# Performance work log

Hardware: AMD Instinct MI355X
Metric: run time of the kernel (lower is better)

Reference implementation:

```python
import jax, jax.numpy as jnp
import numpy as np

NB, BS, NHID, NINP = 6, 200, 1200, 2400  # num_blocks, block_size, nhid, ninp (=2*nhid)
T, B, NTOK = 32, 32, 16000


def _ln(x, g, b):
    mu = x.mean(-1, keepdims=True)
    v = ((x - mu) ** 2).mean(-1, keepdims=True)
    return (x - mu) / jnp.sqrt(v + 1e-5) * g + b


def _attend(q3, k3, v3, wq, wk, wv, wfc, g, b, nh, dk, dv, residual):
    # q3/k3/v3: (B, L, d_model); multi-head scaled-dot attention across blocks
    Bz, L, _ = q3.shape
    qh = (q3 @ wq).reshape(Bz, L, nh, dk)
    kh = (k3 @ wk).reshape(Bz, L, nh, dk)
    vh = (v3 @ wv).reshape(Bz, L, nh, dv)
    att = jnp.einsum('bqhd,bkhd->bhqk', qh, kh) / float(np.sqrt(dk))
    att = jax.nn.softmax(att, axis=-1)
    out = jnp.einsum('bhqk,bkhd->bqhd', att, vh).reshape(Bz, L, nh * dv)
    out = out @ wfc
    if residual:
        out = out + q3
    return _ln(out, g, b)


def setup_inputs() -> dict:
    key = jax.random.key(0)
    ks = jax.random.split(key, 16)
    rn = lambda i, sh, s: jax.random.normal(ks[i], sh, dtype=jnp.float32) * s
    d = {}
    d['tokens'] = jax.random.randint(ks[0], (T, B), 0, NTOK)
    d['h0'] = jnp.zeros((2, B, NHID), jnp.float32)
    d['c0'] = jnp.zeros((2, B, NHID), jnp.float32)
    d['emb_table'] = jax.random.uniform(ks[1], (NTOK, NINP), jnp.float32, -0.1, 0.1)
    d['Wi'] = rn(2, (NB, 4 * BS, NINP), 0.01)
    d['Wh'] = rn(3, (NB, 4 * BS, BS), 0.05)
    d['bih'] = jnp.zeros((NB, 4 * BS), jnp.float32)
    d['bhh'] = jnp.zeros((NB, 4 * BS), jnp.float32)
    d['mq'] = rn(4, (BS, 64), 0.07)
    d['mk'] = rn(5, (BS, 64), 0.07)
    d['mv'] = rn(6, (BS, 64), 0.07)
    d['mfc'] = rn(7, (64, BS), 0.1)
    d['mg'] = jnp.ones((BS,), jnp.float32)
    d['mb'] = jnp.zeros((BS,), jnp.float32)
    d['lq'] = rn(8, (BS, 1600), 0.07)
    d['lk'] = rn(9, (BS, 1600), 0.07)
    d['lv'] = rn(10, (BS, 1600), 0.07)
    d['lfc'] = rn(11, (1600, 2400), 0.02)
    d['lg'] = jnp.ones((2400,), jnp.float32)
    d['lb'] = jnp.zeros((2400,), jnp.float32)
    d['dec_w'] = jax.random.uniform(ks[12], (NTOK, NHID), jnp.float32, -0.1, 0.1)
    d['dec_b'] = jnp.zeros((NTOK,), jnp.float32)
    return d


def reference(tokens, h0, c0, emb_table, Wi, Wh, bih, bhh, mq, mk, mv, mfc, mg, mb,
              lq, lk, lv, lfc, lg, lb, dec_w, dec_b):
    def block_lstm(x, h, c):
        # block-diagonal LSTMCell: k independent cells, per-block input NINP, hidden BS
        Bz = x.shape[0]
        xb = x.reshape(Bz, NB, -1)
        hb = h.reshape(Bz, NB, BS)
        cb = c.reshape(Bz, NB, BS)
        gt = jnp.einsum('bki,kgi->bkg', xb, Wi) + jnp.einsum('bkh,kgh->bkg', hb, Wh) + bih + bhh
        ii, ff, gg, oo = jnp.split(gt, 4, axis=-1)  # torch LSTMCell gate order i,f,g,o
        cn = jax.nn.sigmoid(ff) * cb + jax.nn.sigmoid(ii) * jnp.tanh(gg)
        hn = jax.nn.sigmoid(oo) * jnp.tanh(cn)
        return hn.reshape(Bz, NHID), cn.reshape(Bz, NHID)

    def self_att(h):
        hb = h.reshape(-1, NB, BS)
        hb = _attend(hb, hb, hb, mq, mk, mv, mfc, mg, mb, 4, 16, 16, True)
        return hb.reshape(-1, NHID)

    emb = emb_table[tokens]  # (T, B, NINP)

    def step0(carry, x):
        h, c = carry
        h, c = block_lstm(jnp.tile(x, (1, NB)), h, c)
        h = self_att(h)
        return (h, c), h

    (hf0, cf0), out = jax.lax.scan(step0, (h0[0], c0[0]), emb)

    def step1(carry, x):
        h, c = carry
        q = h.reshape(-1, NB, BS)
        kv = x.reshape(-1, NB, BS)
        inp = _attend(q, kv, kv, lq, lk, lv, lfc, lg, lb, 8, BS, BS, False)  # (B, NB, 2400)
        h, c = block_lstm(inp.reshape(inp.shape[0], -1), h, c)
        h = self_att(h)
        return (h, c), h

    (hf1, cf1), out = jax.lax.scan(step1, (h0[1], c0[1]), out)

    decoded = out @ dec_w.T + dec_b  # (T, B, NTOK)
    return decoded, jnp.stack([hf0, hf1]), jnp.stack([cf0, cf1])
```

## Files before the change

kernel.cpp:

```cpp
#include <hip/hip_runtime.h>
#include <math.h>

#define NBLK 6
#define BS   200
#define NHID 1200
#define NINP 2400
#define TT   32
#define BZ   32
#define NTOK 16000
#define NG   4800
#define ROWS 1024
#define L1D  1600
#define ST   (BZ*NHID)

__device__ __forceinline__ float sigmoidf_(float x) { return 1.0f / (1.0f + expf(-x)); }

template <bool BT>
__global__ __launch_bounds__(256) void gemm128_kernel(
    const float* __restrict__ A, const float* __restrict__ B,
    const float* __restrict__ bias1, const float* __restrict__ bias2,
    float* __restrict__ C, int M, int N, int K, const int* __restrict__ a_idx)
{
    __shared__ __align__(16) float As[8][132];
    __shared__ __align__(16) float Bs[8][132];
    const int tid = threadIdx.x;
    const int tx = tid & 15, ty = tid >> 4;
    const int n0 = blockIdx.x * 128, m0 = blockIdx.y * 128;

    const int la_r = tid >> 1, la_k = (tid & 1) * 4;
    long arow;
    {
        int row = m0 + la_r;
        arow = a_idx ? (long)a_idx[row] * K : (long)row * K;
    }
    float acc[8][8] = {};

    for (int k0 = 0; k0 < K; k0 += 8) {
        {
            float4 v = *(const float4*)&A[arow + k0 + la_k];
            As[la_k + 0][la_r] = v.x;
            As[la_k + 1][la_r] = v.y;
            As[la_k + 2][la_r] = v.z;
            As[la_k + 3][la_r] = v.w;
        }
        if constexpr (!BT) {
            int kk = tid >> 5, n = (tid & 31) * 4;
            int col = n0 + n;
            float4 v = make_float4(0.f, 0.f, 0.f, 0.f);
            if (col < N) v = *(const float4*)&B[(long)(k0 + kk) * N + col];
            *(float4*)&Bs[kk][n] = v;
        } else {
            int n = tid >> 1, kk0 = (tid & 1) * 4;
            int col = n0 + n;
            float4 v = make_float4(0.f, 0.f, 0.f, 0.f);
            if (col < N) v = *(const float4*)&B[(long)col * K + k0 + kk0];
            Bs[kk0 + 0][n] = v.x;
            Bs[kk0 + 1][n] = v.y;
            Bs[kk0 + 2][n] = v.z;
            Bs[kk0 + 3][n] = v.w;
        }
        __syncthreads();
        #pragma unroll
        for (int kk = 0; kk < 8; kk++) {
            float av[8], bv[8];
            *(float4*)&av[0] = *(const float4*)&As[kk][ty * 4];
            *(float4*)&av[4] = *(const float4*)&As[kk][ty * 4 + 64];
            *(float4*)&bv[0] = *(const float4*)&Bs[kk][tx * 4];
            *(float4*)&bv[4] = *(const float4*)&Bs[kk][tx * 4 + 64];
            #pragma unroll
            for (int i = 0; i < 8; i++)
                #pragma unroll
                for (int j = 0; j < 8; j++) acc[i][j] += av[i] * bv[j];
        }
        __syncthreads();
    }
    #pragma unroll
    for (int i = 0; i < 8; i++) {
        int row = m0 + ty * 4 + (i & 3) + (i >> 2) * 64;
        #pragma unroll
        for (int jg = 0; jg < 2; jg++) {
            int col = n0 + tx * 4 + jg * 64;
            if (col < N) {
                float4 v;
                v.x = acc[i][jg * 4 + 0]; v.y = acc[i][jg * 4 + 1];
                v.z = acc[i][jg * 4 + 2]; v.w = acc[i][jg * 4 + 3];
                if (bias1) {
                    float4 b1 = *(const float4*)&bias1[col];
                    v.x += b1.x; v.y += b1.y; v.z += b1.z; v.w += b1.w;
                }
                if (bias2) {
                    float4 b2 = *(const float4*)&bias2[col];
                    v.x += b2.x; v.y += b2.y; v.z += b2.z; v.w += b2.w;
                }
                *(float4*)&C[(long)row * N + col] = v;
            }
        }
    }
}

__global__ __launch_bounds__(256) void gemm_skp_kernel(
    const float* __restrict__ A, const float* __restrict__ B,
    float* __restrict__ Cp, int M, int N, int K, int KL)
{
    __shared__ __align__(16) float As[8][68];
    __shared__ __align__(16) float Bs[8][68];
    const int tid = threadIdx.x;
    const int tx = tid & 15, ty = tid >> 4;
    const int n0 = blockIdx.x * 64, m0 = blockIdx.y * 64;
    const int z = blockIdx.z;
    const int kbeg = z * KL, kend = kbeg + KL;

    float acc[4][4] = {};

    for (int k0 = kbeg; k0 < kend; k0 += 8) {
        {
            int idx = tid * 2;
            int mm = idx >> 3, kk = idx & 7;
            int row = m0 + mm;
            float2 v = *(const float2*)&A[(long)row * K + k0 + kk];
            As[kk][mm] = v.x;
            As[kk + 1][mm] = v.y;
        }
        {
            int idx = tid * 2;
            int nn = idx & 63, kk = idx >> 6;
            int n = n0 + nn;
            float2 v = make_float2(0.f, 0.f);
            if (n < N) v = *(const float2*)&B[(long)(k0 + kk) * N + n];
            Bs[kk][nn] = v.x;
            Bs[kk][nn + 1] = v.y;
        }
        __syncthreads();
        #pragma unroll
        for (int kk = 0; kk < 8; kk++) {
            const float4 a4 = *(const float4*)&As[kk][ty * 4];
            const float4 b4 = *(const float4*)&Bs[kk][tx * 4];
            const float av[4] = {a4.x, a4.y, a4.z, a4.w};
            const float bv[4] = {b4.x, b4.y, b4.z, b4.w};
            #pragma unroll
            for (int i = 0; i < 4; i++)
                #pragma unroll
                for (int j = 0; j < 4; j++) acc[i][j] += av[i] * bv[j];
        }
        __syncthreads();
    }
    float* Cz = Cp + (long)z * M * N;
    #pragma unroll
    for (int i = 0; i < 4; i++) {
        int row = m0 + ty * 4 + i;
        #pragma unroll
        for (int j = 0; j < 4; j++) {
            int col = n0 + tx * 4 + j;
            if (col < N) Cz[(long)row * N + col] = acc[i][j];
        }
    }
}

__global__ __launch_bounds__(256) void bigb_kernel(
    const float* __restrict__ lq, const float* __restrict__ lk,
    float* __restrict__ BigB)
{
    int id = blockIdx.x * 256 + threadIdx.x;
    if (id >= 320000) return;
    int h = id / 40000, r = id % 40000, cp = r / 200, c = r % 200;
    const float4* a = (const float4*)(lq + (long)c * L1D + h * 200);
    const float4* b = (const float4*)(lk + (long)cp * L1D + h * 200);
    float s0 = 0, s1 = 0, s2 = 0, s3 = 0;
    #pragma unroll 5
    for (int d = 0; d < 50; d++) {
        float4 av = a[d], bv = b[d];
        s0 += av.x * bv.x; s1 += av.y * bv.y; s2 += av.z * bv.z; s3 += av.w * bv.w;
    }
    BigB[(long)cp * L1D + h * 200 + c] = s0 + s1 + s2 + s3;
}

__global__ __launch_bounds__(256) void whT_kernel(
    const float* __restrict__ Wh, float* __restrict__ WhT)
{
    int id = blockIdx.x * 256 + threadIdx.x;
    if (id >= 960000) return;
    int k = id / 160000, r = id % 160000, m = r / 800, g = r % 800;
    WhT[id] = Wh[(long)(k * 800 + g) * 200 + m];
}

__device__ __forceinline__ void att_inline(
    float* hb, float* aux, float* gout,
    const float* __restrict__ mq, const float* __restrict__ mk,
    const float* __restrict__ mv, const float* __restrict__ mfc,
    const float* __restrict__ mg, const float* __restrict__ mb)
{
    const int tid = threadIdx.x;
    float* qh   = aux;
    float* kh   = aux + 384;
    float* vh   = aux + 768;
    float* att  = aux + 1152;
    float* outp = aux + 1296;
    float* o2   = aux + 1680;
    float* mu_s = aux + 2880;
    float* rs_s = aux + 2888;
    if (tid < 192) {
        int which = tid >> 6, hd = tid & 63;
        const float* Mw = which == 0 ? mq : (which == 1 ? mk : mv);
        float acc[6] = {};
        for (int jx = 0; jx < 200; jx++) {
            float w = Mw[jx * 64 + hd];
            #pragma unroll
            for (int l = 0; l < 6; l++) acc[l] += hb[l * 200 + jx] * w;
        }
        float* dst = which == 0 ? qh : (which == 1 ? kh : vh);
        #pragma unroll
        for (int l = 0; l < 6; l++) dst[l * 64 + hd] = acc[l];
    }
    __syncthreads();
    if (tid < 144) {
        int h = tid / 36, r = tid % 36, q = r / 6, kk = r % 6;
        float s = 0;
        #pragma unroll
        for (int d = 0; d < 16; d++) s += qh[q * 64 + h * 16 + d] * kh[kk * 64 + h * 16 + d];
        att[(h * 6 + q) * 6 + kk] = s * 0.25f;
    }
    __syncthreads();
    if (tid < 24) {
        float* a = att + tid * 6;
        float mx = a[0];
        for (int i = 1; i < 6; i++) mx = fmaxf(mx, a[i]);
        float sm = 0;
        for (int i = 0; i < 6; i++) { a[i] = expf(a[i] - mx); sm += a[i]; }
        float inv = 1.f / sm;
        for (int i = 0; i < 6; i++) a[i] *= inv;
    }
    __syncthreads();
    for (int id = tid; id < 384; id += 256) {
        int q = id >> 6, hd = id & 63, h = hd >> 4;
        float s = 0;
        #pragma unroll
        for (int kk = 0; kk < 6; kk++) s += att[(h * 6 + q) * 6 + kk] * vh[kk * 64 + hd];
        outp[id] = s;
    }
    __syncthreads();
    if (tid < 200) {
        float acc[6] = {};
        for (int d = 0; d < 64; d++) {
            float w = mfc[d * 200 + tid];
            #pragma unroll
            for (int q = 0; q < 6; q++) acc[q] += outp[q * 64 + d] * w;
        }
        #pragma unroll
        for (int q = 0; q < 6; q++) o2[q * 200 + tid] = acc[q] + hb[q * 200 + tid];
    }
    __syncthreads();
    if (tid < 6) {
        const float4* o4 = (const float4*)(o2 + tid * 200);
        float s = 0, s2 = 0;
        for (int i = 0; i < 50; i++) {
            float4 v = o4[i];
            s += v.x + v.y + v.z + v.w;
            s2 += v.x * v.x + v.y * v.y + v.z * v.z + v.w * v.w;
        }
        float mu = s / 200.f;
        float var = s2 / 200.f - mu * mu;
        mu_s[tid] = mu;
        rs_s[tid] = 1.0f / sqrtf(var + 1e-5f);
    }
    __syncthreads();
    for (int i = tid; i < 300; i += 256) {
        int q = i / 50;
        float4 v = ((float4*)o2)[i];
        float4 g4 = ((const float4*)mg)[i % 50];
        float4 b4 = ((const float4*)mb)[i % 50];
        float mu = mu_s[q], rstd = rs_s[q];
        float4 r;
        r.x = (v.x - mu) * rstd * g4.x + b4.x;
        r.y = (v.y - mu) * rstd * g4.y + b4.y;
        r.z = (v.z - mu) * rstd * g4.z + b4.z;
        r.w = (v.w - mu) * rstd * g4.w + b4.w;
        ((float4*)hb)[i] = r;
        if (gout) ((float4*)(gout))[i] = r;
    }
    __syncthreads();
}

__global__ __launch_bounds__(256) void phaseA_kernel(
    const float* __restrict__ GX0, const float* __restrict__ h0,
    const float* __restrict__ c0, const float* __restrict__ WhT,
    float* __restrict__ out0, float* __restrict__ cf0,
    const float* __restrict__ mq, const float* __restrict__ mk,
    const float* __restrict__ mv, const float* __restrict__ mfc,
    const float* __restrict__ mg, const float* __restrict__ mb)
{
    __shared__ __align__(16) float h_s[1200];
    __shared__ __align__(16) float c_s[1200];
    __shared__ __align__(16) float g_s[4800];
    __shared__ __align__(16) float gx_s[4800];
    __shared__ __align__(16) float aux[2896];
    const int b = blockIdx.x, tid = threadIdx.x;
    for (int i = tid; i < 300; i += 256) {
        ((float4*)h_s)[i] = ((const float4*)(h0 + b * NHID))[i];
        ((float4*)c_s)[i] = ((const float4*)(c0 + b * NHID))[i];
    }
    __syncthreads();
    for (int t = 0; t < TT; t++) {
        const float4* gx4 = (const float4*)(GX0 + ((long)t * BZ + b) * NG);
        for (int i = tid; i < 1200; i += 256) ((float4*)gx_s)[i] = gx4[i];
        if (tid < 200) {
            #pragma unroll
            for (int k = 0; k < 6; k++) {
                const float* wp = WhT + (long)k * 160000 + tid * 4;
                float a0 = 0, a1 = 0, a2 = 0, a3 = 0;
                for (int m = 0; m < 200; m++) {
                    float hv = h_s[k * 200 + m];
                    float4 w = *(const float4*)(wp + (long)m * 800);
                    a0 += hv * w.x; a1 += hv * w.y; a2 += hv * w.z; a3 += hv * w.w;
                }
                int gb = k * 800 + tid * 4;
                g_s[gb] = a0; g_s[gb + 1] = a1; g_s[gb + 2] = a2; g_s[gb + 3] = a3;
            }
        }
        __syncthreads();
        for (int idx = tid; idx < 1200; idx += 256) {
            int k = idx / 200, j = idx - k * 200;
            int base = k * 800 + j;
            float gi = g_s[base] + gx_s[base];
            float gf = g_s[base + 200] + gx_s[base + 200];
            float gg = g_s[base + 400] + gx_s[base + 400];
            float go = g_s[base + 600] + gx_s[base + 600];
            float cn = sigmoidf_(gf) * c_s[idx] + sigmoidf_(gi) * tanhf(gg);
            c_s[idx] = cn;
            h_s[idx] = sigmoidf_(go) * tanhf(cn);
        }
        __syncthreads();
        att_inline(h_s, aux, out0 + (long)t * ST + b * NHID, mq, mk, mv, mfc, mg, mb);
    }
    for (int i = tid; i < 300; i += 256)
        ((float4*)(cf0 + b * NHID))[i] = ((float4*)c_s)[i];
}

template <bool FIRST>
__global__ __launch_bounds__(256) void fusedatt_kernel(
    const float* __restrict__ htmp, const float* __restrict__ h0l1,
    float* __restrict__ out1_prev,
    const float* __restrict__ KMt, const float* __restrict__ VHt,
    float* __restrict__ attV,
    const float* __restrict__ mq, const float* __restrict__ mk,
    const float* __restrict__ mv, const float* __restrict__ mfc,
    const float* __restrict__ mg, const float* __restrict__ mb)
{
    __shared__ __align__(16) float hb[1200];
    __shared__ __align__(16) float aux[2896];
    __shared__ float attp[72];
    __shared__ float attr[36];
    const int blk = blockIdx.x, b = blk >> 3, h = blk & 7, tid = threadIdx.x;
    if (FIRST) {
        for (int i = tid; i < 300; i += 256)
            ((float4*)hb)[i] = ((const float4*)(h0l1 + b * NHID))[i];
        __syncthreads();
    } else {
        for (int i = tid; i < 300; i += 256)
            ((float4*)hb)[i] = ((const float4*)(htmp + b * NHID))[i];
        __syncthreads();
        att_inline(hb, aux, (h == 0) ? out1_prev + b * NHID : nullptr,
                   mq, mk, mv, mfc, mg, mb);
    }
    const float* kb = KMt + (long)b * 9600 + h * 200;
    if (tid < 72) {
        int r = tid >> 1, half = tid & 1;
        int q = r / 6, kk = r % 6;
        const float4* qr = (const float4*)(hb + q * 200 + half * 100);
        const float4* kr = (const float4*)(kb + (long)kk * L1D + half * 100);
        float s0 = 0, s1 = 0, s2 = 0, s3 = 0;
        #pragma unroll 5
        for (int d = 0; d < 25; d++) {
            float4 a = qr[d], v = kr[d];
            s0 += a.x * v.x; s1 += a.y * v.y; s2 += a.z * v.z; s3 += a.w * v.w;
        }
        attp[tid] = s0 + s1 + s2 + s3;
    }
    __syncthreads();
    if (tid < 6) {
        float v[6]; float mx = -1e30f;
        #pragma unroll
        for (int kk = 0; kk < 6; kk++) {
            float s = (attp[(tid * 6 + kk) * 2] + attp[(tid * 6 + kk) * 2 + 1]) * 0.07071067811865475f;
            v[kk] = s; mx = fmaxf(mx, s);
        }
        float sm = 0;
        #pragma unroll
        for (int kk = 0; kk < 6; kk++) { v[kk] = expf(v[kk] - mx); sm += v[kk]; }
        float inv = 1.f / sm;
        #pragma unroll
        for (int kk = 0; kk < 6; kk++) attr[tid * 6 + kk] = v[kk] * inv;
    }
    __syncthreads();
    if (tid < 200) {
        int hd = h * 200 + tid;
        const float* vb = VHt + (long)b * 9600 + hd;
        float v0 = vb[0], v1 = vb[L1D], v2 = vb[2 * L1D];
        float v3 = vb[3 * L1D], v4 = vb[4 * L1D], v5 = vb[5 * L1D];
        #pragma unroll
        for (int q = 0; q < 6; q++) {
            const float* a = attr + q * 6;
            attV[(long)b * 9600 + q * L1D + hd] =
                a[0] * v0 + a[1] * v1 + a[2] * v2 + a[3] * v3 + a[4] * v4 + a[5] * v5;
        }
    }
}

__global__ __launch_bounds__(256) void attsmall_kernel(
    const float* __restrict__ h_in, float* __restrict__ h_out,
    const float* __restrict__ mq, const float* __restrict__ mk,
    const float* __restrict__ mv, const float* __restrict__ mfc,
    const float* __restrict__ mg, const float* __restrict__ mb)
{
    __shared__ __align__(16) float hb[1200];
    __shared__ __align__(16) float aux[2896];
    const int b = blockIdx.x, tid = threadIdx.x;
    for (int i = tid; i < 300; i += 256)
        ((float4*)hb)[i] = ((const float4*)(h_in + b * NHID))[i];
    __syncthreads();
    att_inline(hb, aux, h_out + b * NHID, mq, mk, mv, mfc, mg, mb);
}

__global__ __launch_bounds__(256) void ln_sum8_kernel(
    const float* __restrict__ Fp, float* __restrict__ Y,
    const float* __restrict__ g, const float* __restrict__ bta)
{
    __shared__ float rowbuf[2400];
    __shared__ float aw[4], bw[4];
    const int r = blockIdx.x, tid = threadIdx.x;
    const long SL = (long)192 * NINP / 4;
    const float4* f0 = (const float4*)(Fp) + (long)r * (NINP / 4);
    float s = 0, s2 = 0;
    for (int i = tid; i < 600; i += 256) {
        float4 v = f0[i];
        #pragma unroll
        for (int z = 1; z < 8; z++) {
            float4 a = f0[(long)z * SL + i];
            v.x += a.x; v.y += a.y; v.z += a.z; v.w += a.w;
        }
        ((float4*)rowbuf)[i] = v;
        s += v.x + v.y + v.z + v.w;
        s2 += v.x * v.x + v.y * v.y + v.z * v.z + v.w * v.w;
    }
    for (int off = 32; off; off >>= 1) { s += __shfl_down(s, off); s2 += __shfl_down(s2, off); }
    int wid = tid >> 6, lane = tid & 63;
    if (lane == 0) { aw[wid] = s; bw[wid] = s2; }
    __syncthreads();
    if (tid == 0) {
        float a = 0, a2 = 0;
        for (int w = 0; w < 4; w++) { a += aw[w]; a2 += bw[w]; }
        float mu = a / NINP;
        float var = a2 / NINP - mu * mu;
        aw[0] = mu;
        bw[0] = 1.0f / sqrtf(var + 1e-5f);
    }
    __syncthreads();
    float mu = aw[0], rstd = bw[0];
    for (int i = tid; i < 600; i += 256) {
        float4 v = ((float4*)rowbuf)[i];
        float4 g4 = ((const float4*)g)[i];
        float4 b4 = ((const float4*)bta)[i];
        float4 o;
        o.x = (v.x - mu) * rstd * g4.x + b4.x;
        o.y = (v.y - mu) * rstd * g4.y + b4.y;
        o.z = (v.z - mu) * rstd * g4.z + b4.z;
        o.w = (v.w - mu) * rstd * g4.w + b4.w;
        ((float4*)(Y + (long)r * NINP))[i] = o;
    }
}

__global__ __launch_bounds__(512) void lstm1_kernel(
    const float* __restrict__ inp, const float* __restrict__ hprev,
    float* __restrict__ c_io, const float* __restrict__ Wi,
    const float* __restrict__ Wh, const float* __restrict__ bih,
    const float* __restrict__ bhh, float* __restrict__ h_out)
{
    __shared__ float h_s[200 * 33];
    __shared__ float x_s[2][100 * 33];
    __shared__ float ps[12][128];
    const int k = blockIdx.y, jt = blockIdx.x, tid = threadIdx.x;
    const int b = tid & 31, jg = (tid >> 5) & 3, kh = tid >> 7;
    const int j = jt * 4 + jg;

    for (int idx = tid; idx < 1600; idx += 512) {
        int bb = idx / 50, m4 = idx % 50;
        float4 v = *(const float4*)&hprev[bb * NHID + k * BS + m4 * 4];
        h_s[(m4 * 4 + 0) * 33 + bb] = v.x;
        h_s[(m4 * 4 + 1) * 33 + bb] = v.y;
        h_s[(m4 * 4 + 2) * 33 + bb] = v.z;
        h_s[(m4 * 4 + 3) * 33 + bb] = v.w;
    }
    for (int idx = tid; idx < 800; idx += 512) {
        int bb = idx / 25, m4 = idx % 25;
        float4 v = *(const float4*)&inp[(long)(bb * 6 + k) * NINP + m4 * 4];
        x_s[0][(m4 * 4 + 0) * 33 + bb] = v.x;
        x_s[0][(m4 * 4 + 1) * 33 + bb] = v.y;
        x_s[0][(m4 * 4 + 2) * 33 + bb] = v.z;
        x_s[0][(m4 * 4 + 3) * 33 + bb] = v.w;
    }

    const float* wi0 = Wi + (long)(k * 800 + j) * NINP;
    const float* wi1 = wi0 + (long)200 * NINP;
    const float* wi2 = wi0 + (long)400 * NINP;
// ... 26 lines not shown
                float x2 = xs[(m + 2) * 33 + b], x3 = xs[(m + 3) * 33 + b];
                a0 += x0 * w0.x + x1 * w0.y + x2 * w0.z + x3 * w0.w;
                a1 += x0 * w1.x + x1 * w1.y + x2 * w1.z + x3 * w1.w;
                a2 += x0 * w2.x + x1 * w2.y + x2 * w2.z + x3 * w2.w;
                a3 += x0 * w3.x + x1 * w3.y + x2 * w3.z + x3 * w3.w;
            }
        }
        cur ^= 1;
    }
    if (kh == 0) {
        const float* w0 = Wh + (long)(k * 800 + j) * 200;
        const float* w1 = w0 + 200 * 200;
        const float* w2 = w0 + 400 * 200;
        const float* w3 = w0 + 600 * 200;
        for (int m = 0; m < 200; m += 4) {
            float4 wv0 = *(const float4*)&w0[m];
            float4 wv1 = *(const float4*)&w1[m];
            float4 wv2 = *(const float4*)&w2[m];
            float4 wv3 = *(const float4*)&w3[m];
            float h0v = h_s[(m + 0) * 33 + b], h1v = h_s[(m + 1) * 33 + b];
            float h2v = h_s[(m + 2) * 33 + b], h3v = h_s[(m + 3) * 33 + b];
            a0 += h0v * wv0.x + h1v * wv0.y + h2v * wv0.z + h3v * wv0.w;
            a1 += h0v * wv1.x + h1v * wv1.y + h2v * wv1.z + h3v * wv1.w;
            a2 += h0v * wv2.x + h1v * wv2.y + h2v * wv2.z + h3v * wv2.w;
            a3 += h0v * wv3.x + h1v * wv3.y + h2v * wv3.z + h3v * wv3.w;
        }
    } else {
        int g = (kh - 1) * 4, t2 = tid & 127;
        ps[g + 0][t2] = a0; ps[g + 1][t2] = a1; ps[g + 2][t2] = a2; ps[g + 3][t2] = a3;
    }
    __syncthreads();
    if (kh == 0) {
        a0 += ps[0][tid] + ps[4][tid] + ps[8][tid];
        a1 += ps[1][tid] + ps[5][tid] + ps[9][tid];
        a2 += ps[2][tid] + ps[6][tid] + ps[10][tid];
        a3 += ps[3][tid] + ps[7][tid] + ps[11][tid];
        int nb2 = k * 800;
        float gi = a0 + bih[nb2 + j] + bhh[nb2 + j];
        float gf = a1 + bih[nb2 + 200 + j] + bhh[nb2 + 200 + j];
        float gg = a2 + bih[nb2 + 400 + j] + bhh[nb2 + 400 + j];
        float go = a3 + bih[nb2 + 600 + j] + bhh[nb2 + 600 + j];
        int o = b * NHID + k * BS + j;
        float cold = c_io[o];
        float cn = sigmoidf_(gf) * cold + sigmoidf_(gi) * tanhf(gg);
        float hn = sigmoidf_(go) * tanhf(cn);
        c_io[o] = cn;
        h_out[o] = hn;
    }
}

extern "C" void kernel_launch(void* const* d_in, const int* in_sizes, int n_in,
                              void* d_out, int out_size, void* d_ws, size_t ws_size,
                              hipStream_t stream)
{
    const int*   tokens = (const int*)  d_in[0];
    const float* h0     = (const float*)d_in[1];
    const float* c0     = (const float*)d_in[2];
    const float* emb    = (const float*)d_in[3];
    const float* Wi     = (const float*)d_in[4];
    const float* Wh     = (const float*)d_in[5];
    const float* bih    = (const float*)d_in[6];
    const float* bhh    = (const float*)d_in[7];
    const float* mq     = (const float*)d_in[8];
    const float* mk     = (const float*)d_in[9];
    const float* mv     = (const float*)d_in[10];
    const float* mfc    = (const float*)d_in[11];
    const float* mg     = (const float*)d_in[12];
    const float* mb     = (const float*)d_in[13];
    const float* lq     = (const float*)d_in[14];
    const float* lk     = (const float*)d_in[15];
    const float* lv     = (const float*)d_in[16];
    const float* lfc    = (const float*)d_in[17];
    const float* lg     = (const float*)d_in[18];
    const float* lb     = (const float*)d_in[19];
    const float* dec_w  = (const float*)d_in[20];
    const float* dec_b  = (const float*)d_in[21];
    float* out = (float*)d_out;

    float* p = (float*)d_ws;
    float* GX0  = p; p += (long)ROWS * NG;
    float* out0 = p; p += (long)ROWS * NHID;
    float* out1 = p; p += (long)ROWS * NHID;
    float* KM   = p; p += (long)ROWS * 6 * L1D;
    float* VH1  = p; p += (long)ROWS * 6 * L1D;
    float* attV = p; p += 192 * L1D;
    float* FCp  = p; p += (long)8 * 192 * NINP;
    float* inp  = p; p += 192 * NINP;
    float* htmp = p; p += BZ * NHID;
    float* cb1  = p; p += BZ * NHID;
    float* BigB = p; p += 200 * L1D;
    float* WhT  = p; p += 6 * 200 * 800;

    long off = (long)ROWS * NTOK;
    float* cf0 = out + off + 2 * ST;

    hipMemcpyAsync(cb1, c0 + ST, ST * sizeof(float), hipMemcpyDeviceToDevice, stream);

    bigb_kernel<<<1250, 256, 0, stream>>>(lq, lk, BigB);
    whT_kernel<<<3750, 256, 0, stream>>>(Wh, WhT);

    gemm128_kernel<true><<<dim3(NG / 128 + 1, ROWS / 128), 256, 0, stream>>>(
        emb, Wi, bih, bhh, GX0, ROWS, NG, NINP, tokens);

    phaseA_kernel<<<BZ, 256, 0, stream>>>(
        GX0, h0, c0, WhT, out0, cf0, mq, mk, mv, mfc, mg, mb);

    gemm128_kernel<false><<<dim3((L1D + 127) / 128, (ROWS * 6) / 128), 256, 0, stream>>>(
        out0, BigB, nullptr, nullptr, KM, ROWS * 6, L1D, BS, nullptr);
    gemm128_kernel<false><<<dim3((L1D + 127) / 128, (ROWS * 6) / 128), 256, 0, stream>>>(
        out0, lv, nullptr, nullptr, VH1, ROWS * 6, L1D, BS, nullptr);

    for (int t = 0; t < TT; t++) {
        const float* hp = (t == 0) ? h0 + ST : out1 + (long)(t - 1) * ST;
        const float* KMt = KM + (long)t * BZ * 6 * L1D;
        const float* VHt = VH1 + (long)t * BZ * 6 * L1D;
        if (t == 0) {
            fusedatt_kernel<true><<<256, 256, 0, stream>>>(
                nullptr, h0 + ST, nullptr, KMt, VHt, attV, mq, mk, mv, mfc, mg, mb);
        } else {
            fusedatt_kernel<false><<<256, 256, 0, stream>>>(
                htmp, nullptr, out1 + (long)(t - 1) * ST, KMt, VHt, attV,
                mq, mk, mv, mfc, mg, mb);
        }
        gemm_skp_kernel<<<dim3((NINP + 63) / 64, 3, 8), 256, 0, stream>>>(
            attV, lfc, FCp, 192, NINP, L1D, 200);
        ln_sum8_kernel<<<192, 256, 0, stream>>>(FCp, inp, lg, lb);
        lstm1_kernel<<<dim3(50, 6), 512, 0, stream>>>(inp, hp, cb1, Wi, Wh, bih, bhh, htmp);
    }
    attsmall_kernel<<<BZ, 256, 0, stream>>>(htmp, out1 + (long)31 * ST, mq, mk, mv, mfc, mg, mb);

    gemm128_kernel<true><<<dim3(NTOK / 128, ROWS / 128), 256, 0, stream>>>(
        out1, dec_w, dec_b, nullptr, out, ROWS, NTOK, NHID, nullptr);

    hipMemcpyAsync(out + off,          out0 + (long)31 * ST, ST * sizeof(float), hipMemcpyDeviceToDevice, stream);
    hipMemcpyAsync(out + off + ST,     out1 + (long)31 * ST, ST * sizeof(float), hipMemcpyDeviceToDevice, stream);
    hipMemcpyAsync(out + off + 3 * ST, cb1,                  ST * sizeof(float), hipMemcpyDeviceToDevice, stream);
}
```

Baseline: 10.64 ms.

## Fuse lfc projection into attention kernel and widen phaseA to 1024 threads

The per-step split-K GEMM for the layer-1 output projection is folded into fusedatt_kernel: each (batch, head) block keeps its attended values in shared memory and multiplies them directly by the matching 200-row slice of lfc, writing per-head partials for ln_sum8. This removes one kernel launch per timestep and the attV round trip through global memory. Separately, the phaseA recurrent kernel goes from 256 to 1024 threads, splitting the Wh dot product into two halves across more threads and reading GX0 directly instead of staging it in shared memory. The trade-off is lower parallelism for the lfc product (256 blocks each reading a 200x2400 slice) and heavier per-block register and shared-memory use.

```diff
diff --git a/kernel.cpp b/kernel.cpp
--- a/kernel.cpp
+++ b/kernel.cpp
@@ -98,64 +98,6 @@
     }
 }
 
-__global__ __launch_bounds__(256) void gemm_skp_kernel(
-    const float* __restrict__ A, const float* __restrict__ B,
-    float* __restrict__ Cp, int M, int N, int K, int KL)
-{
-    __shared__ __align__(16) float As[8][68];
-    __shared__ __align__(16) float Bs[8][68];
-    const int tid = threadIdx.x;
-    const int tx = tid & 15, ty = tid >> 4;
-    const int n0 = blockIdx.x * 64, m0 = blockIdx.y * 64;
-    const int z = blockIdx.z;
-    const int kbeg = z * KL, kend = kbeg + KL;
-
-    float acc[4][4] = {};
-
-    for (int k0 = kbeg; k0 < kend; k0 += 8) {
-        {
-            int idx = tid * 2;
-            int mm = idx >> 3, kk = idx & 7;
-            int row = m0 + mm;
-            float2 v = *(const float2*)&A[(long)row * K + k0 + kk];
-            As[kk][mm] = v.x;
-            As[kk + 1][mm] = v.y;
-        }
-        {
-            int idx = tid * 2;
-            int nn = idx & 63, kk = idx >> 6;
-            int n = n0 + nn;
-            float2 v = make_float2(0.f, 0.f);
-            if (n < N) v = *(const float2*)&B[(long)(k0 + kk) * N + n];
-            Bs[kk][nn] = v.x;
-            Bs[kk][nn + 1] = v.y;
-        }
-        __syncthreads();
-        #pragma unroll
-        for (int kk = 0; kk < 8; kk++) {
-            const float4 a4 = *(const float4*)&As[kk][ty * 4];
-            const float4 b4 = *(const float4*)&Bs[kk][tx * 4];
-            const float av[4] = {a4.x, a4.y, a4.z, a4.w};
-            const float bv[4] = {b4.x, b4.y, b4.z, b4.w};
-            #pragma unroll
-            for (int i = 0; i < 4; i++)
-                #pragma unroll
-                for (int j = 0; j < 4; j++) acc[i][j] += av[i] * bv[j];
-        }
-        __syncthreads();
-    }
-    float* Cz = Cp + (long)z * M * N;
-    #pragma unroll
-    for (int i = 0; i < 4; i++) {
-        int row = m0 + ty * 4 + i;
-        #pragma unroll
-        for (int j = 0; j < 4; j++) {
-            int col = n0 + tx * 4 + j;
-            if (col < N) Cz[(long)row * N + col] = acc[i][j];
-        }
-    }
-}
-
 __global__ __launch_bounds__(256) void bigb_kernel(
     const float* __restrict__ lq, const float* __restrict__ lk,
     float* __restrict__ BigB)
@@ -183,6 +125,7 @@
     WhT[id] = Wh[(long)(k * 800 + g) * 200 + m];
 }
 
+template <int NT>
 __device__ __forceinline__ void att_inline(
     float* hb, float* aux, float* gout,
     const float* __restrict__ mq, const float* __restrict__ mk,
@@ -230,7 +173,7 @@
         for (int i = 0; i < 6; i++) a[i] *= inv;
     }
     __syncthreads();
-    for (int id = tid; id < 384; id += 256) {
+    for (int id = tid; id < 384; id += NT) {
         int q = id >> 6, hd = id & 63, h = hd >> 4;
         float s = 0;
         #pragma unroll
@@ -263,7 +206,7 @@
         rs_s[tid] = 1.0f / sqrtf(var + 1e-5f);
     }
     __syncthreads();
-    for (int i = tid; i < 300; i += 256) {
+    for (int i = tid; i < 300; i += NT) {
         int q = i / 50;
         float4 v = ((float4*)o2)[i];
         float4 g4 = ((const float4*)mg)[i % 50];
@@ -280,7 +223,7 @@
     __syncthreads();
 }
 
-__global__ __launch_bounds__(256) void phaseA_kernel(
+__global__ __launch_bounds__(1024) void phaseA_kernel(
     const float* __restrict__ GX0, const float* __restrict__ h0,
     const float* __restrict__ c0, const float* __restrict__ WhT,
     float* __restrict__ out0, float* __restrict__ cf0,
@@ -291,47 +234,48 @@
     __shared__ __align__(16) float h_s[1200];
     __shared__ __align__(16) float c_s[1200];
     __shared__ __align__(16) float g_s[4800];
-    __shared__ __align__(16) float gx_s[4800];
-    __shared__ __align__(16) float aux[2896];
+    __shared__ __align__(16) float ps[4800];
     const int b = blockIdx.x, tid = threadIdx.x;
-    for (int i = tid; i < 300; i += 256) {
+    for (int i = tid; i < 300; i += 1024) {
         ((float4*)h_s)[i] = ((const float4*)(h0 + b * NHID))[i];
         ((float4*)c_s)[i] = ((const float4*)(c0 + b * NHID))[i];
     }
     __syncthreads();
     for (int t = 0; t < TT; t++) {
-        const float4* gx4 = (const float4*)(GX0 + ((long)t * BZ + b) * NG);
-        for (int i = tid; i < 1200; i += 256) ((float4*)gx_s)[i] = gx4[i];
-        if (tid < 200) {
-            #pragma unroll
-            for (int k = 0; k < 6; k++) {
-                const float* wp = WhT + (long)k * 160000 + tid * 4;
-                float a0 = 0, a1 = 0, a2 = 0, a3 = 0;
-                for (int m = 0; m < 200; m++) {
-                    float hv = h_s[k * 200 + m];
-                    float4 w = *(const float4*)(wp + (long)m * 800);
-                    a0 += hv * w.x; a1 += hv * w.y; a2 += hv * w.z; a3 += hv * w.w;
-                }
-                int gb = k * 800 + tid * 4;
-                g_s[gb] = a0; g_s[gb + 1] = a1; g_s[gb + 2] = a2; g_s[gb + 3] = a3;
+        for (int tau = tid; tau < 2400; tau += 1024) {
+            int mh = (tau >= 1200);
+            int slot = tau - mh * 1200;
+            int k = slot / 200, g4 = slot - k * 200;
+            const float* wp = WhT + (long)k * 160000 + (long)mh * 80000 + g4 * 4;
+            const float* hp2 = h_s + k * 200 + mh * 100;
+            float a0 = 0, a1 = 0, a2 = 0, a3 = 0;
+            #pragma unroll 4
+            for (int m = 0; m < 100; m++) {
+                float hv = hp2[m];
+                float4 w = *(const float4*)(wp + (long)m * 800);
+                a0 += hv * w.x; a1 += hv * w.y; a2 += hv * w.z; a3 += hv * w.w;
             }
+            float* dst = mh ? ps : g_s;
+            int o = k * 800 + g4 * 4;
+            dst[o] = a0; dst[o + 1] = a1; dst[o + 2] = a2; dst[o + 3] = a3;
         }
         __syncthreads();
-        for (int idx = tid; idx < 1200; idx += 256) {
+        const float* gxp = GX0 + ((long)t * BZ + b) * NG;
+        for (int idx = tid; idx < 1200; idx += 1024) {
             int k = idx / 200, j = idx - k * 200;
             int base = k * 800 + j;
-            float gi = g_s[base] + gx_s[base];
-            float gf = g_s[base + 200] + gx_s[base + 200];
-            float gg = g_s[base + 400] + gx_s[base + 400];
-            float go = g_s[base + 600] + gx_s[base + 600];
+            float gi = g_s[base]       + ps[base]       + gxp[base];
+            float gf = g_s[base + 200] + ps[base + 200] + gxp[base + 200];
+            float gg = g_s[base + 400] + ps[base + 400] + gxp[base + 400];
+            float go = g_s[base + 600] + ps[base + 600] + gxp[base + 600];
             float cn = sigmoidf_(gf) * c_s[idx] + sigmoidf_(gi) * tanhf(gg);
             c_s[idx] = cn;
             h_s[idx] = sigmoidf_(go) * tanhf(cn);
         }
         __syncthreads();
-        att_inline(h_s, aux, out0 + (long)t * ST + b * NHID, mq, mk, mv, mfc, mg, mb);
-    }
-    for (int i = tid; i < 300; i += 256)
+        att_inline<1024>(h_s, ps, out0 + (long)t * ST + b * NHID, mq, mk, mv, mfc, mg, mb);
+    }
+    for (int i = tid; i < 300; i += 1024)
         ((float4*)(cf0 + b * NHID))[i] = ((float4*)c_s)[i];
 }
 
@@ -340,13 +284,14 @@
     const float* __restrict__ htmp, const float* __restrict__ h0l1,
     float* __restrict__ out1_prev,
     const float* __restrict__ KMt, const float* __restrict__ VHt,
-    float* __restrict__ attV,
+    const float* __restrict__ lfc, float* __restrict__ Fp,
     const float* __restrict__ mq, const float* __restrict__ mk,
     const float* __restrict__ mv, const float* __restrict__ mfc,
     const float* __restrict__ mg, const float* __restrict__ mb)
 {
     __shared__ __align__(16) float hb[1200];
     __shared__ __align__(16) float aux[2896];
+    __shared__ __align__(16) float a_s[1200];
     __shared__ float attp[72];
     __shared__ float attr[36];
     const int blk = blockIdx.x, b = blk >> 3, h = blk & 7, tid = threadIdx.x;
@@ -358,8 +303,8 @@
         for (int i = tid; i < 300; i += 256)
             ((float4*)hb)[i] = ((const float4*)(htmp + b * NHID))[i];
         __syncthreads();
-        att_inline(hb, aux, (h == 0) ? out1_prev + b * NHID : nullptr,
-                   mq, mk, mv, mfc, mg, mb);
+        att_inline<256>(hb, aux, (h == 0) ? out1_prev + b * NHID : nullptr,
+                        mq, mk, mv, mfc, mg, mb);
     }
     const float* kb = KMt + (long)b * 9600 + h * 200;
     if (tid < 72) {
@@ -399,9 +344,27 @@
         #pragma unroll
         for (int q = 0; q < 6; q++) {
             const float* a = attr + q * 6;
-            attV[(long)b * 9600 + q * L1D + hd] =
+            a_s[q * 200 + tid] =
                 a[0] * v0 + a[1] * v1 + a[2] * v2 + a[3] * v3 + a[4] * v4 + a[5] * v5;
         }
+    }
+    __syncthreads();
+    const float4* lfc4 = (const float4*)lfc;
+    for (int c4 = tid; c4 < 600; c4 += 256) {
+        float4 acc[6] = {};
+        #pragma unroll 2
+        for (int m = 0; m < 200; m++) {
+            float4 w = lfc4[(long)(h * 200 + m) * 600 + c4];
+            #pragma unroll
+            for (int q = 0; q < 6; q++) {
+                float a = a_s[q * 200 + m];
+                acc[q].x += a * w.x; acc[q].y += a * w.y;
+                acc[q].z += a * w.z; acc[q].w += a * w.w;
+            }
+        }
+        #pragma unroll
+        for (int q = 0; q < 6; q++)
+            *(float4*)&Fp[((long)h * 192 + b * 6 + q) * NINP + c4 * 4] = acc[q];
     }
 }
 
@@ -417,7 +380,7 @@
     for (int i = tid; i < 300; i += 256)
         ((float4*)hb)[i] = ((const float4*)(h_in + b * NHID))[i];
     __syncthreads();
-    att_inline(hb, aux, h_out + b * NHID, mq, mk, mv, mfc, mg, mb);
+    att_inline<256>(hb, aux, h_out + b * NHID, mq, mk, mv, mfc, mg, mb);
 }
 
 __global__ __launch_bounds__(256) void ln_sum8_kernel(
@@ -611,7 +574,6 @@
     float* out1 = p; p += (long)ROWS * NHID;
     float* KM   = p; p += (long)ROWS * 6 * L1D;
     float* VH1  = p; p += (long)ROWS * 6 * L1D;
-    float* attV = p; p += 192 * L1D;
     float* FCp  = p; p += (long)8 * 192 * NINP;
     float* inp  = p; p += 192 * NINP;
     float* htmp = p; p += BZ * NHID;
@@ -630,7 +592,7 @@
     gemm128_kernel<true><<<dim3(NG / 128 + 1, ROWS / 128), 256, 0, stream>>>(
         emb, Wi, bih, bhh, GX0, ROWS, NG, NINP, tokens);
 
-    phaseA_kernel<<<BZ, 256, 0, stream>>>(
+    phaseA_kernel<<<BZ, 1024, 0, stream>>>(
         GX0, h0, c0, WhT, out0, cf0, mq, mk, mv, mfc, mg, mb);
 
     gemm128_kernel<false><<<dim3((L1D + 127) / 128, (ROWS * 6) / 128), 256, 0, stream>>>(
@@ -644,14 +606,12 @@
         const float* VHt = VH1 + (long)t * BZ * 6 * L1D;
         if (t == 0) {
             fusedatt_kernel<true><<<256, 256, 0, stream>>>(
-                nullptr, h0 + ST, nullptr, KMt, VHt, attV, mq, mk, mv, mfc, mg, mb);
+                nullptr, h0 + ST, nullptr, KMt, VHt, lfc, FCp, mq, mk, mv, mfc, mg, mb);
         } else {
             fusedatt_kernel<false><<<256, 256, 0, stream>>>(
-                htmp, nullptr, out1 + (long)(t - 1) * ST, KMt, VHt, attV,
+                htmp, nullptr, out1 + (long)(t - 1) * ST, KMt, VHt, lfc, FCp,
                 mq, mk, mv, mfc, mg, mb);
         }
-        gemm_skp_kernel<<<dim3((NINP + 63) / 64, 3, 8), 256, 0, stream>>>(
-            attV, lfc, FCp, 192, NINP, L1D, 200);
         ln_sum8_kernel<<<192, 256, 0, stream>>>(FCp, inp, lg, lb);
         lstm1_kernel<<<dim3(50, 6), 512, 0, stream>>>(inp, hp, cb1, Wi, Wh, bih, bhh, htmp);
     }
```

Result: slower. 12.56 ms (+18.0%).

## Precompose value and output projections to remove per-step FC GEMM; widen phase-A block

Applied to the files above, without the earlier changes.

Folds the layer-1 attention value projection with the output FC (lv@lfc per head), then precomputes per-timestep per-head projected values for all rows. Each recurrent step now needs only a single fused kernel (scores, softmax, weighted sum over precomputed values, LayerNorm) instead of attention, split-K GEMM and LN-sum kernels. Phase A is also widened to 1024 threads and its Wh matvec is split across two half-K partial sums. The trade is a large extra workspace and a heavy precompute GEMM (8x the value data), with a fallback to the old path when workspace is too small.

```diff
diff --git a/kernel.cpp b/kernel.cpp
--- a/kernel.cpp
+++ b/kernel.cpp
@@ -98,6 +98,73 @@
     }
 }
 
+__global__ __launch_bounds__(256) void gemmz_kernel(
+    const float* __restrict__ A, const float* __restrict__ B, float* __restrict__ C,
+    int M, int N, int K,
+    long a_rstride, long a_zoff, long b_zoff, long c_rstride, long c_zoff)
+{
+    __shared__ __align__(16) float As[8][132];
+    __shared__ __align__(16) float Bs[8][132];
+    const int tid = threadIdx.x;
+    const int tx = tid & 15, ty = tid >> 4;
+    const int n0 = blockIdx.x * 128, m0 = blockIdx.y * 128;
+    const int z = blockIdx.z;
+    const float* Az = A + a_zoff * z;
+    const float* Bz = B + b_zoff * z;
+    float* Cz = C + c_zoff * z;
+
+    const int la_r = tid >> 1, la_k = (tid & 1) * 4;
+    int arow_i = m0 + la_r; if (arow_i >= M) arow_i = M - 1;
+    const long arow = (long)arow_i * a_rstride;
+    float acc[8][8] = {};
+
+    for (int k0 = 0; k0 < K; k0 += 8) {
+        {
+            float4 v = *(const float4*)&Az[arow + k0 + la_k];
+            As[la_k + 0][la_r] = v.x;
+            As[la_k + 1][la_r] = v.y;
+            As[la_k + 2][la_r] = v.z;
+            As[la_k + 3][la_r] = v.w;
+        }
+        {
+            int kk = tid >> 5, n = (tid & 31) * 4;
+            int col = n0 + n;
+            float4 v = make_float4(0.f, 0.f, 0.f, 0.f);
+            if (col < N) v = *(const float4*)&Bz[(long)(k0 + kk) * N + col];
+            *(float4*)&Bs[kk][n] = v;
+        }
+        __syncthreads();
+        #pragma unroll
+        for (int kk = 0; kk < 8; kk++) {
+            float av[8], bv[8];
+            *(float4*)&av[0] = *(const float4*)&As[kk][ty * 4];
+            *(float4*)&av[4] = *(const float4*)&As[kk][ty * 4 + 64];
+            *(float4*)&bv[0] = *(const float4*)&Bs[kk][tx * 4];
+            *(float4*)&bv[4] = *(const float4*)&Bs[kk][tx * 4 + 64];
+            #pragma unroll
+            for (int i = 0; i < 8; i++)
+                #pragma unroll
+                for (int j = 0; j < 8; j++) acc[i][j] += av[i] * bv[j];
+        }
+        __syncthreads();
+    }
+    #pragma unroll
+    for (int i = 0; i < 8; i++) {
+        int row = m0 + ty * 4 + (i & 3) + (i >> 2) * 64;
+        if (row >= M) continue;
+        #pragma unroll
+        for (int jg = 0; jg < 2; jg++) {
+            int col = n0 + tx * 4 + jg * 64;
+            if (col < N) {
+                float4 v;
+                v.x = acc[i][jg * 4 + 0]; v.y = acc[i][jg * 4 + 1];
+                v.z = acc[i][jg * 4 + 2]; v.w = acc[i][jg * 4 + 3];
+                *(float4*)&Cz[(long)row * c_rstride + col] = v;
+            }
+        }
+    }
+}
+
 __global__ __launch_bounds__(256) void gemm_skp_kernel(
     const float* __restrict__ A, const float* __restrict__ B,
     float* __restrict__ Cp, int M, int N, int K, int KL)
@@ -183,6 +250,7 @@
     WhT[id] = Wh[(long)(k * 800 + g) * 200 + m];
 }
 
+template <int NT>
 __device__ __forceinline__ void att_inline(
     float* hb, float* aux, float* gout,
     const float* __restrict__ mq, const float* __restrict__ mk,
@@ -230,7 +298,7 @@
         for (int i = 0; i < 6; i++) a[i] *= inv;
     }
     __syncthreads();
-    for (int id = tid; id < 384; id += 256) {
+    for (int id = tid; id < 384; id += NT) {
         int q = id >> 6, hd = id & 63, h = hd >> 4;
         float s = 0;
         #pragma unroll
@@ -263,7 +331,7 @@
         rs_s[tid] = 1.0f / sqrtf(var + 1e-5f);
     }
     __syncthreads();
-    for (int i = tid; i < 300; i += 256) {
+    for (int i = tid; i < 300; i += NT) {
         int q = i / 50;
         float4 v = ((float4*)o2)[i];
         float4 g4 = ((const float4*)mg)[i % 50];
@@ -280,7 +348,7 @@
     __syncthreads();
 }
 
-__global__ __launch_bounds__(256) void phaseA_kernel(
+__global__ __launch_bounds__(1024) void phaseA_kernel(
     const float* __restrict__ GX0, const float* __restrict__ h0,
     const float* __restrict__ c0, const float* __restrict__ WhT,
     float* __restrict__ out0, float* __restrict__ cf0,
@@ -291,52 +359,184 @@
     __shared__ __align__(16) float h_s[1200];
     __shared__ __align__(16) float c_s[1200];
     __shared__ __align__(16) float g_s[4800];
-    __shared__ __align__(16) float gx_s[4800];
-    __shared__ __align__(16) float aux[2896];
+    __shared__ __align__(16) float ps[4800];
     const int b = blockIdx.x, tid = threadIdx.x;
-    for (int i = tid; i < 300; i += 256) {
+    for (int i = tid; i < 300; i += 1024) {
         ((float4*)h_s)[i] = ((const float4*)(h0 + b * NHID))[i];
         ((float4*)c_s)[i] = ((const float4*)(c0 + b * NHID))[i];
     }
     __syncthreads();
     for (int t = 0; t < TT; t++) {
-        const float4* gx4 = (const float4*)(GX0 + ((long)t * BZ + b) * NG);
-        for (int i = tid; i < 1200; i += 256) ((float4*)gx_s)[i] = gx4[i];
-        if (tid < 200) {
-            #pragma unroll
-            for (int k = 0; k < 6; k++) {
-                const float* wp = WhT + (long)k * 160000 + tid * 4;
-                float a0 = 0, a1 = 0, a2 = 0, a3 = 0;
-                for (int m = 0; m < 200; m++) {
-                    float hv = h_s[k * 200 + m];
-                    float4 w = *(const float4*)(wp + (long)m * 800);
-                    a0 += hv * w.x; a1 += hv * w.y; a2 += hv * w.z; a3 += hv * w.w;
-                }
-                int gb = k * 800 + tid * 4;
-                g_s[gb] = a0; g_s[gb + 1] = a1; g_s[gb + 2] = a2; g_s[gb + 3] = a3;
-            }
-        }
-        __syncthreads();
-        for (int idx = tid; idx < 1200; idx += 256) {
+        for (int tau = tid; tau < 2400; tau += 1024) {
+            int mh = (tau >= 1200);
+            int slot = tau - mh * 1200;
+            int k = slot / 200, g4 = slot - k * 200;
+            const float* wp = WhT + (long)k * 160000 + (long)mh * 80000 + g4 * 4;
+            const float* hp2 = h_s + k * 200 + mh * 100;
+            float a0 = 0, a1 = 0, a2 = 0, a3 = 0;
+            float e0 = 0, e1 = 0, e2 = 0, e3 = 0;
+            #pragma unroll 4
+            for (int m = 0; m < 100; m += 2) {
+                float hv0 = hp2[m], hv1 = hp2[m + 1];
+                float4 w0 = *(const float4*)(wp + (long)m * 800);
+                float4 w1 = *(const float4*)(wp + (long)m * 800 + 800);
+                a0 += hv0 * w0.x; a1 += hv0 * w0.y; a2 += hv0 * w0.z; a3 += hv0 * w0.w;
+                e0 += hv1 * w1.x; e1 += hv1 * w1.y; e2 += hv1 * w1.z; e3 += hv1 * w1.w;
+            }
+            float* dst = mh ? ps : g_s;
+            int o = k * 800 + g4 * 4;
+            dst[o] = a0 + e0; dst[o + 1] = a1 + e1;
+            dst[o + 2] = a2 + e2; dst[o + 3] = a3 + e3;
+        }
+        __syncthreads();
+        const float* gxp = GX0 + ((long)t * BZ + b) * NG;
+        for (int idx = tid; idx < 1200; idx += 1024) {
             int k = idx / 200, j = idx - k * 200;
             int base = k * 800 + j;
-            float gi = g_s[base] + gx_s[base];
-            float gf = g_s[base + 200] + gx_s[base + 200];
-            float gg = g_s[base + 400] + gx_s[base + 400];
-            float go = g_s[base + 600] + gx_s[base + 600];
+            float gi = g_s[base]       + ps[base]       + gxp[base];
+            float gf = g_s[base + 200] + ps[base + 200] + gxp[base + 200];
+            float gg = g_s[base + 400] + ps[base + 400] + gxp[base + 400];
+            float go = g_s[base + 600] + ps[base + 600] + gxp[base + 600];
             float cn = sigmoidf_(gf) * c_s[idx] + sigmoidf_(gi) * tanhf(gg);
             c_s[idx] = cn;
             h_s[idx] = sigmoidf_(go) * tanhf(cn);
         }
         __syncthreads();
-        att_inline(h_s, aux, out0 + (long)t * ST + b * NHID, mq, mk, mv, mfc, mg, mb);
-    }
-    for (int i = tid; i < 300; i += 256)
+        att_inline<1024>(h_s, ps, out0 + (long)t * ST + b * NHID, mq, mk, mv, mfc, mg, mb);
+    }
+    for (int i = tid; i < 300; i += 1024)
         ((float4*)(cf0 + b * NHID))[i] = ((float4*)c_s)[i];
 }
 
 template <bool FIRST>
-__global__ __launch_bounds__(256) void fusedatt_kernel(
+__global__ __launch_bounds__(512) void fusedatt_vfh_kernel(
+    const float* __restrict__ hraw, float* __restrict__ out1_prev,
+    const float* __restrict__ KMt, const float* __restrict__ VFht,
+    float* __restrict__ inp, const float* __restrict__ lg, const float* __restrict__ lbta,
+    const float* __restrict__ mq, const float* __restrict__ mk,
+    const float* __restrict__ mv, const float* __restrict__ mfc,
+    const float* __restrict__ mg, const float* __restrict__ mb)
+{
+    __shared__ __align__(16) float hb[1200];
+    __shared__ __align__(16) float aux[2896];
+    __shared__ float attp[288];
+    __shared__ float aw[8][6], bw[8][6], mu_s[6], rs_s[6];
+    const int b = blockIdx.x, tid = threadIdx.x;
+    for (int i = tid; i < 300; i += 512)
+        ((float4*)hb)[i] = ((const float4*)(hraw + b * NHID))[i];
+    __syncthreads();
+    if (!FIRST)
+        att_inline<512>(hb, aux, out1_prev + b * NHID, mq, mk, mv, mfc, mg, mb);
+
+    if (tid < 288) {
+        int h = tid / 36, r = tid % 36, q = r / 6, kk = r % 6;
+        const float4* qr = (const float4*)(hb + q * 200);
+        const float4* kr = (const float4*)(KMt + ((long)(b * 6 + kk)) * L1D + h * 200);
+        float s0 = 0, s1 = 0, s2 = 0, s3 = 0;
+        #pragma unroll 5
+        for (int d = 0; d < 50; d++) {
+            float4 a = qr[d], v = kr[d];
+            s0 += a.x * v.x; s1 += a.y * v.y; s2 += a.z * v.z; s3 += a.w * v.w;
+        }
+        attp[(h * 6 + q) * 6 + kk] = (s0 + s1 + s2 + s3) * 0.07071067811865475f;
+    }
+    __syncthreads();
+    if (tid < 48) {
+        float* a = attp + tid * 6;
+        float mx = a[0];
+        for (int i = 1; i < 6; i++) mx = fmaxf(mx, a[i]);
+        float sm = 0;
+        for (int i = 0; i < 6; i++) { a[i] = expf(a[i] - mx); sm += a[i]; }
+        float inv = 1.f / sm;
+        for (int i = 0; i < 6; i++) a[i] *= inv;
+    }
+    __syncthreads();
+
+    float fa0[5] = {}, fa1[5] = {}, fa2[5] = {}, fa3[5] = {}, fa4[5] = {}, fa5[5] = {};
+    const float* vbase = VFht + (long)b * 48 * NINP;
+    #pragma unroll 1
+    for (int kk = 0; kk < 6; kk++) {
+        #pragma unroll 1
+        for (int h = 0; h < 8; h++) {
+            const float* vb = vbase + (long)(kk * 8 + h) * NINP;
+            float w0 = attp[(h * 6 + 0) * 6 + kk];
+            float w1 = attp[(h * 6 + 1) * 6 + kk];
+            float w2 = attp[(h * 6 + 2) * 6 + kk];
+            float w3 = attp[(h * 6 + 3) * 6 + kk];
+            float w4 = attp[(h * 6 + 4) * 6 + kk];
+            float w5 = attp[(h * 6 + 5) * 6 + kk];
+            float v[5];
+            #pragma unroll
+            for (int i = 0; i < 5; i++) {
+                int c = tid + (i << 9);
+                v[i] = (c < NINP) ? vb[c] : 0.f;
+            }
+            #pragma unroll
+            for (int i = 0; i < 5; i++) {
+                fa0[i] += w0 * v[i]; fa1[i] += w1 * v[i]; fa2[i] += w2 * v[i];
+                fa3[i] += w3 * v[i]; fa4[i] += w4 * v[i]; fa5[i] += w5 * v[i];
+            }
+        }
+    }
+    {
+        float s[6] = {}, s2[6] = {};
+        #pragma unroll
+        for (int i = 0; i < 5; i++) {
+            s[0] += fa0[i]; s2[0] += fa0[i] * fa0[i];
+            s[1] += fa1[i]; s2[1] += fa1[i] * fa1[i];
+            s[2] += fa2[i]; s2[2] += fa2[i] * fa2[i];
+            s[3] += fa3[i]; s2[3] += fa3[i] * fa3[i];
+            s[4] += fa4[i]; s2[4] += fa4[i] * fa4[i];
+            s[5] += fa5[i]; s2[5] += fa5[i] * fa5[i];
+        }
+        #pragma unroll
+        for (int off = 32; off; off >>= 1) {
+            #pragma unroll
+            for (int q = 0; q < 6; q++) {
+                s[q] += __shfl_down(s[q], off);
+                s2[q] += __shfl_down(s2[q], off);
+            }
+        }
+        int wid = tid >> 6, lane = tid & 63;
+        if (lane == 0) {
+            #pragma unroll
+            for (int q = 0; q < 6; q++) { aw[wid][q] = s[q]; bw[wid][q] = s2[q]; }
+        }
+    }
+    __syncthreads();
+    if (tid < 6) {
+        float a = 0, a2 = 0;
+        #pragma unroll
+        for (int w = 0; w < 8; w++) { a += aw[w][tid]; a2 += bw[w][tid]; }
+        float mu = a / NINP;
+        float var = a2 / NINP - mu * mu;
+        mu_s[tid] = mu;
+        rs_s[tid] = 1.0f / sqrtf(var + 1e-5f);
+    }
+    __syncthreads();
+    {
+        float mu0 = mu_s[0], r0 = rs_s[0], mu1 = mu_s[1], r1 = rs_s[1];
+        float mu2 = mu_s[2], r2 = rs_s[2], mu3 = mu_s[3], r3 = rs_s[3];
+        float mu4 = mu_s[4], r4 = rs_s[4], mu5 = mu_s[5], r5 = rs_s[5];
+        #pragma unroll
+        for (int i = 0; i < 5; i++) {
+            int c = tid + (i << 9);
+            if (c < NINP) {
+                float g = lg[c], be = lbta[c];
+                long rb = (long)(b * 6) * NINP + c;
+                inp[rb]             = (fa0[i] - mu0) * r0 * g + be;
+                inp[rb + NINP]      = (fa1[i] - mu1) * r1 * g + be;
+                inp[rb + 2 * NINP]  = (fa2[i] - mu2) * r2 * g + be;
+                inp[rb + 3 * NINP]  = (fa3[i] - mu3) * r3 * g + be;
+                inp[rb + 4 * NINP]  = (fa4[i] - mu4) * r4 * g + be;
+                inp[rb + 5 * NINP]  = (fa5[i] - mu5) * r5 * g + be;
+            }
+        }
+    }
+}
+
+template <bool FIRST>
+__global__ __launch_bounds__(256) void fusedatt_fb_kernel(
     const float* __restrict__ htmp, const float* __restrict__ h0l1,
     float* __restrict__ out1_prev,
     const float* __restrict__ KMt, const float* __restrict__ VHt,
@@ -358,8 +558,8 @@
         for (int i = tid; i < 300; i += 256)
             ((float4*)hb)[i] = ((const float4*)(htmp + b * NHID))[i];
         __syncthreads();
-        att_inline(hb, aux, (h == 0) ? out1_prev + b * NHID : nullptr,
-                   mq, mk, mv, mfc, mg, mb);
+        att_inline<256>(hb, aux, (h == 0) ? out1_prev + b * NHID : nullptr,
+                        mq, mk, mv, mfc, mg, mb);
     }
     const float* kb = KMt + (long)b * 9600 + h * 200;
     if (tid < 72) {
@@ -417,7 +617,7 @@
     for (int i = tid; i < 300; i += 256)
         ((float4*)hb)[i] = ((const float4*)(h_in + b * NHID))[i];
     __syncthreads();
-    att_inline(hb, aux, h_out + b * NHID, mq, mk, mv, mfc, mg, mb);
+    att_inline<256>(hb, aux, h_out + b * NHID, mq, mk, mv, mfc, mg, mb);
 }
 
 __global__ __launch_bounds__(256) void ln_sum8_kernel(
@@ -610,14 +810,16 @@
     float* out0 = p; p += (long)ROWS * NHID;
     float* out1 = p; p += (long)ROWS * NHID;
     float* KM   = p; p += (long)ROWS * 6 * L1D;
-    float* VH1  = p; p += (long)ROWS * 6 * L1D;
-    float* attV = p; p += 192 * L1D;
-    float* FCp  = p; p += (long)8 * 192 * NINP;
     float* inp  = p; p += 192 * NINP;
     float* htmp = p; p += BZ * NHID;
     float* cb1  = p; p += BZ * NHID;
     float* BigB = p; p += 200 * L1D;
     float* WhT  = p; p += 6 * 200 * 800;
+    long common = p - (float*)d_ws;
+    const long LVF_SZ = (long)8 * 200 * NINP;
+    const long VFH_SZ = (long)ROWS * 6 * 8 * NINP;
+    const bool use_vfh =
+        ws_size >= (size_t)(common + LVF_SZ + VFH_SZ + 1024) * sizeof(float);
 
     long off = (long)ROWS * NTOK;
     float* cf0 = out + off + 2 * ST;
@@ -630,31 +832,64 @@
     gemm128_kernel<true><<<dim3(NG / 128 + 1, ROWS / 128), 256, 0, stream>>>(
         emb, Wi, bih, bhh, GX0, ROWS, NG, NINP, tokens);
 
-    phaseA_kernel<<<BZ, 256, 0, stream>>>(
+    phaseA_kernel<<<BZ, 1024, 0, stream>>>(
         GX0, h0, c0, WhT, out0, cf0, mq, mk, mv, mfc, mg, mb);
 
     gemm128_kernel<false><<<dim3((L1D + 127) / 128, (ROWS * 6) / 128), 256, 0, stream>>>(
         out0, BigB, nullptr, nullptr, KM, ROWS * 6, L1D, BS, nullptr);
-    gemm128_kernel<false><<<dim3((L1D + 127) / 128, (ROWS * 6) / 128), 256, 0, stream>>>(
-        out0, lv, nullptr, nullptr, VH1, ROWS * 6, L1D, BS, nullptr);
-
-    for (int t = 0; t < TT; t++) {
-        const float* hp = (t == 0) ? h0 + ST : out1 + (long)(t - 1) * ST;
-        const float* KMt = KM + (long)t * BZ * 6 * L1D;
-        const float* VHt = VH1 + (long)t * BZ * 6 * L1D;
-        if (t == 0) {
-            fusedatt_kernel<true><<<256, 256, 0, stream>>>(
-                nullptr, h0 + ST, nullptr, KMt, VHt, attV, mq, mk, mv, mfc, mg, mb);
-        } else {
-            fusedatt_kernel<false><<<256, 256, 0, stream>>>(
-                htmp, nullptr, out1 + (long)(t - 1) * ST, KMt, VHt, attV,
-                mq, mk, mv, mfc, mg, mb);
-        }
-        gemm_skp_kernel<<<dim3((NINP + 63) / 64, 3, 8), 256, 0, stream>>>(
-            attV, lfc, FCp, 192, NINP, L1D, 200);
-        ln_sum8_kernel<<<192, 256, 0, stream>>>(FCp, inp, lg, lb);
-        lstm1_kernel<<<dim3(50, 6), 512, 0, stream>>>(inp, hp, cb1, Wi, Wh, bih, bhh, htmp);
-    }
+
+    if (use_vfh) {
+        float* LVF = p;
+        float* VFh = p + LVF_SZ;
+        gemmz_kernel<<<dim3((NINP + 127) / 128, 2, 8), 256, 0, stream>>>(
+            lv, lfc, LVF, 200, NINP, 200,
+            (long)L1D, 200L, (long)200 * NINP, (long)NINP, (long)200 * NINP);
+        gemmz_kernel<<<dim3((NINP + 127) / 128, (ROWS * 6) / 128, 8), 256, 0, stream>>>(
+            out0, LVF, VFh, ROWS * 6, NINP, 200,
+            200L, 0L, (long)200 * NINP, (long)8 * NINP, (long)NINP);
+
+        for (int t = 0; t < TT; t++) {
+            const float* hp = (t == 0) ? h0 + ST : out1 + (long)(t - 1) * ST;
+            const float* KMt = KM + (long)t * BZ * 6 * L1D;
+            const float* VFht = VFh + (long)t * BZ * 6 * 8 * NINP;
+            if (t == 0) {
+                fusedatt_vfh_kernel<true><<<BZ, 512, 0, stream>>>(
+                    h0 + ST, nullptr, KMt, VFht, inp, lg, lb,
+                    mq, mk, mv, mfc, mg, mb);
+            } else {
+                fusedatt_vfh_kernel<false><<<BZ, 512, 0, stream>>>(
+                    htmp, out1 + (long)(t - 1) * ST, KMt, VFht, inp, lg, lb,
+                    mq, mk, mv, mfc, mg, mb);
+            }
+            lstm1_kernel<<<dim3(50, 6), 512, 0, stream>>>(
+                inp, hp, cb1, Wi, Wh, bih, bhh, htmp);
+        }
+    } else {
+        float* VH1  = p;
+        float* attV = VH1 + (long)ROWS * 6 * L1D;
+        float* FCp  = attV + 192 * L1D;
+        gemm128_kernel<false><<<dim3((L1D + 127) / 128, (ROWS * 6) / 128), 256, 0, stream>>>(
+            out0, lv, nullptr, nullptr, VH1, ROWS * 6, L1D, BS, nullptr);
+        for (int t = 0; t < TT; t++) {
+            const float* hp = (t == 0) ? h0 + ST : out1 + (long)(t - 1) * ST;
+            const float* KMt = KM + (long)t * BZ * 6 * L1D;
+            const float* VHt = VH1 + (long)t * BZ * 6 * L1D;
+            if (t == 0) {
+                fusedatt_fb_kernel<true><<<256, 256, 0, stream>>>(
+                    nullptr, h0 + ST, nullptr, KMt, VHt, attV, mq, mk, mv, mfc, mg, mb);
+            } else {
+                fusedatt_fb_kernel<false><<<256, 256, 0, stream>>>(
+                    htmp, nullptr, out1 + (long)(t - 1) * ST, KMt, VHt, attV,
+                    mq, mk, mv, mfc, mg, mb);
+            }
+            gemm_skp_kernel<<<dim3((NINP + 63) / 64, 3, 8), 256, 0, stream>>>(
+                attV, lfc, FCp, 192, NINP, L1D, 200);
+            ln_sum8_kernel<<<192, 256, 0, stream>>>(FCp, inp, lg, lb);
+            lstm1_kernel<<<dim3(50, 6), 512, 0, stream>>>(
+                inp, hp, cb1, Wi, Wh, bih, bhh, htmp);
+        }
+    }
+
     attsmall_kernel<<<BZ, 256, 0, stream>>>(htmp, out1 + (long)31 * ST, mq, mk, mv, mfc, mg, mb);
 
     gemm128_kernel<true><<<dim3(NTOK / 128, ROWS / 128), 256, 0, stream>>>(
```

Measured after the change: 11.00 ms. +3.3%, slower.
